# Kernel tuning notes

Measured on AMD Instinct MI355X. Metric: run time of the kernel, lower is better.

Reference implementation:

```python
import jax, jax.numpy as jnp
import numpy as np

BATCH, SEQ, D_MODEL, D_STATE = 16, 1024, 512, 32
DT_MIN, DT_MAX, DT_FLOOR = 1e-3, 1e-1, 1e-4


def _init_ssm(key):
    k1, k2, k3, k4 = jax.random.split(key, 4)
    scale = 1.0 / np.sqrt(D_STATE)
    z = jax.random.normal(k1, (D_MODEL, D_STATE)) * scale
    A_log = -jnp.exp(z)  # A = exp(A_log) in (0,1)
    B = jax.random.normal(k2, (D_MODEL, D_STATE)) * scale
    C = jax.random.normal(k3, (D_MODEL, D_STATE)) * scale
    log_dt = jax.random.uniform(k4, (D_MODEL,)) * (np.log(DT_MAX) - np.log(DT_MIN)) + np.log(DT_MIN)
    log_dt = jnp.maximum(log_dt, np.log(DT_FLOOR))
    return A_log, B, C, log_dt


def setup_inputs() -> dict:
    key = jax.random.key(0)
    kx, khr, kbr = jax.random.split(key, 3)
    x = jax.random.normal(kx, (BATCH, SEQ, D_MODEL), dtype=jnp.float32)
    A_log_hr, B_hr, C_hr, log_dt_hr = _init_ssm(khr)
    A_log_br, B_br, C_br, log_dt_br = _init_ssm(kbr)
    return dict(
        x=x,
        A_log_hr=A_log_hr, B_hr=B_hr, C_hr=C_hr, log_dt_hr=log_dt_hr,
        A_log_br=A_log_br, B_br=B_br, C_br=C_br, log_dt_br=log_dt_br,
        weight_hr=jnp.ones((D_MODEL,), jnp.float32),
        weight_br=jnp.ones((D_MODEL,), jnp.float32),
    )


def _ssm(x, A_log, B, C, log_dt):
    # delta=None path: dt = exp(log_dt) * dt_scale(=1), time-invariant -> dA, dB are [d, n]
    dt = jnp.exp(log_dt)                 # [d]
    A = jnp.exp(A_log)                   # [d, n]
    dA = jnp.exp(dt[:, None] * A)        # [d, n]  (matches torch: exp(dt*exp(A_log)))
    dB = dt[:, None] * B                 # [d, n]
    b = x.shape[0]
    h0 = jnp.zeros((b, A.shape[0], A.shape[1]), x.dtype)  # [b, d, n]

    def step(h, xt):  # xt: [b, d]
        h = dA * h + dB * xt[:, :, None]
        y = jnp.einsum('bdn,dn->bd', h, C)
        return h, y

    _, ys = jax.lax.scan(step, h0, jnp.swapaxes(x, 0, 1))  # ys: [L, b, d]
    return jnp.swapaxes(ys, 0, 1)        # [b, L, d]


def reference(x, A_log_hr, B_hr, C_hr, log_dt_hr,
              A_log_br, B_br, C_br, log_dt_br,
              weight_hr, weight_br):
    x_hr = _ssm(x, A_log_hr, B_hr, C_hr, log_dt_hr) * weight_hr  # [b, L, d]
    x_br = _ssm(x, A_log_br, B_br, C_br, log_dt_br) * weight_br
    return (x_hr, x_br, x_hr + x_br)  # hr_enhanced, br_enhanced, combined
```

## Files before the change

kernel.cpp:

```cpp
#include <hip/hip_runtime.h>

#define BATCH 16
#define SEQ   1024
#define DM    512
#define NST   32
#define PF    8

#define PIN(v) asm volatile("" : "+v"(v))


__global__ __launch_bounds__(256) void ssm_pass1(
    const float* __restrict__ x,
    const float* __restrict__ Alog_hr, const float* __restrict__ ldt_hr,
    const float* __restrict__ Alog_br, const float* __restrict__ ldt_br,
    float* __restrict__ E, int nc, int cl)
{
    int tid  = threadIdx.x;
    int dlo  = tid & 127;
    int nh   = tid >> 7;
    int bid  = blockIdx.x;
    int dblk = bid & 3;
    int r    = bid >> 2;
    int ncm1 = nc - 1;
    int c    = r % ncm1;  r /= ncm1;
    int b    = r & (BATCH - 1);
    int ssm  = r >> 4;
    int d    = dblk * 128 + dlo;
    int n0   = nh * 16;

    const float* Alog = ssm ? Alog_br : Alog_hr;
    const float* ldt  = ssm ? ldt_br  : ldt_hr;

    float dt = expf(ldt[d]);
    float dA[16], g[16];
#pragma unroll
    for (int i = 0; i < 16; ++i) {
        dA[i] = expf(dt * expf(Alog[d * NST + n0 + i]));
        g[i]  = 0.f;
    }
#pragma unroll
    for (int i = 0; i < 16; ++i) PIN(dA[i]);

    const float* xp = x + ((size_t)b * SEQ + (size_t)c * cl) * DM + d;

    float xf[PF];
#pragma unroll
    for (int k = 0; k < PF; ++k) xf[k] = xp[(size_t)k * DM];
    const float* xq = xp + (size_t)PF * DM;

    int ntb = cl / PF;
    for (int t8 = 0; t8 < ntb - 1; ++t8) {
#pragma unroll
        for (int j = 0; j < PF; ++j) {
            float xv = xf[j];
            xf[j] = xq[(size_t)j * DM];
#pragma unroll
            for (int i = 0; i < 16; ++i) g[i] = fmaf(dA[i], g[i], xv);
        }
        xq += (size_t)PF * DM;
    }
#pragma unroll
    for (int j = 0; j < PF; ++j) {
        float xv = xf[j];
#pragma unroll
        for (int i = 0; i < 16; ++i) g[i] = fmaf(dA[i], g[i], xv);
    }

    float* sp = E + ((((size_t)ssm * BATCH + b) * nc + c) * NST + n0) * DM + d;
#pragma unroll
    for (int i = 0; i < 16; ++i) sp[(size_t)i * DM] = g[i];
}

__global__ __launch_bounds__(128, 2) void ssm_pass3(
    const float* __restrict__ x,
    const float* __restrict__ Alog_hr, const float* __restrict__ B_hr,
    const float* __restrict__ C_hr,    const float* __restrict__ ldt_hr,
    const float* __restrict__ Alog_br, const float* __restrict__ B_br,
    const float* __restrict__ C_br,    const float* __restrict__ ldt_br,
    const float* __restrict__ w_hr,    const float* __restrict__ w_br,
    const float* __restrict__ E,
    float* __restrict__ out_hr, float* __restrict__ out_br, float* __restrict__ out_cb,
    int nc, int cl)
{
    int tid  = threadIdx.x;
    int lane = tid & 63;
    int wid  = tid >> 6;
    int ssm  = lane >> 5;
    int dlo  = lane & 31;
    int bid  = blockIdx.x;
    int dblk = bid & 7;
    int r    = bid >> 3;
    int c    = r % nc;
    int b    = r / nc;
    int d    = dblk * 64 + wid * 32 + dlo;

    const float* Alog = ssm ? Alog_br : Alog_hr;
    const float* Bm   = ssm ? B_br    : B_hr;
    const float* Cm   = ssm ? C_br    : C_hr;
    const float* ldt  = ssm ? ldt_br  : ldt_hr;
    const float* w    = ssm ? w_br    : w_hr;

    float dt = expf(ldt[d]);
    float wd = w[d];

    float A[NST], g[NST];
#pragma unroll
    for (int n = 0; n < NST; ++n) {
        A[n] = expf(Alog[d * NST + n]);
        g[n] = 0.f;
    }
    {
        float p[NST];
#pragma unroll
        for (int n = 0; n < NST; ++n) p[n] = expf((float)cl * dt * A[n]);
        const size_t slab = (size_t)NST * DM;
        const float* ep = E + (((size_t)ssm * BATCH + b) * nc) * slab + d;
        for (int cc = 0; cc < c; ++cc) {
#pragma unroll
            for (int n = 0; n < NST; ++n)
                g[n] = fmaf(p[n], g[n], ep[(size_t)n * DM]);
            ep += slab;
        }
    }

    float dA[NST], Cw[NST];
#pragma unroll
    for (int n = 0; n < NST; ++n) {
        dA[n] = expf(dt * A[n]);
        Cw[n] = Cm[d * NST + n] * Bm[d * NST + n] * dt * wd;
    }
#pragma unroll
    for (int n = 0; n < NST; ++n) { PIN(dA[n]); PIN(Cw[n]); }

    size_t off = ((size_t)b * SEQ + (size_t)c * cl) * DM + d;
    const float* xp = x + off;
    float* oh = out_hr + off;
    float* ob = out_br + off;
    float* oc = out_cb + off;

    float xf[PF];
#pragma unroll
    for (int k = 0; k < PF; ++k) xf[k] = xp[(size_t)k * DM];
    const float* xq = xp + (size_t)PF * DM;

#define BODY(xv)                                                        \
    {                                                                   \
        float y0 = 0.f, y1 = 0.f, y2 = 0.f, y3 = 0.f;                   \
        _Pragma("unroll")                                               \
        for (int n = 0; n < NST; n += 4) {                              \
            g[n]     = fmaf(dA[n],     g[n],     xv);                   \
            g[n + 1] = fmaf(dA[n + 1], g[n + 1], xv);                   \
            g[n + 2] = fmaf(dA[n + 2], g[n + 2], xv);                   \
            g[n + 3] = fmaf(dA[n + 3], g[n + 3], xv);                   \
            y0 = fmaf(Cw[n],     g[n],     y0);                         \
            y1 = fmaf(Cw[n + 1], g[n + 1], y1);                         \
            y2 = fmaf(Cw[n + 2], g[n + 2], y2);                         \
            y3 = fmaf(Cw[n + 3], g[n + 3], y3);                         \
        }                                                               \
        float y  = (y0 + y1) + (y2 + y3);                               \
        float yo = __shfl_xor(y, 32, 64);                               \
        if (ssm == 0) { *oh = y; *oc = y + yo; }                        \
        else          { *ob = y; }                                      \
        oh += DM;  ob += DM;  oc += DM;                                 \
    }

    int ntb = cl / PF;
    for (int t8 = 0; t8 < ntb - 1; ++t8) {
#pragma unroll
        for (int j = 0; j < PF; ++j) {
            float xv = xf[j];
            xf[j] = xq[(size_t)j * DM];
            BODY(xv);
        }
        xq += (size_t)PF * DM;
    }
#pragma unroll
    for (int j = 0; j < PF; ++j) {
        float xv = xf[j];
        BODY(xv);
    }
#undef BODY
}

extern "C" void kernel_launch(void* const* d_in, const int* in_sizes, int n_in,
                              void* d_out, int out_size, void* d_ws, size_t ws_size,
                              hipStream_t stream)
{
    (void)in_sizes; (void)n_in; (void)out_size;

    const float* x       = (const float*)d_in[0];
    const float* Alog_hr = (const float*)d_in[1];
    const float* B_hr    = (const float*)d_in[2];
    const float* C_hr    = (const float*)d_in[3];
    const float* ldt_hr  = (const float*)d_in[4];
    const float* Alog_br = (const float*)d_in[5];
    const float* B_br    = (const float*)d_in[6];
    const float* C_br    = (const float*)d_in[7];
    const float* ldt_br  = (const float*)d_in[8];
    const float* w_hr    = (const float*)d_in[9];
    const float* w_br    = (const float*)d_in[10];

    float* out    = (float*)d_out;
    const size_t one = (size_t)BATCH * SEQ * DM;
    float* out_hr = out;
    float* out_br = out + one;
    float* out_cb = out + 2 * one;

    float* E = (float*)d_ws;

    int nc = 8;
    while (nc > 1 &&
           ws_size < (size_t)2 * BATCH * nc * NST * DM * sizeof(float))
        nc >>= 1;
    int cl = SEQ / nc;

    if (nc > 1) {
        int nblk1 = 2 * BATCH * (nc - 1) * 4;
        ssm_pass1<<<nblk1, 256, 0, stream>>>(x, Alog_hr, ldt_hr, Alog_br, ldt_br,
                                             E, nc, cl);
    }

    int nblk3 = BATCH * nc * 8;
    ssm_pass3<<<nblk3, 128, 0, stream>>>(x,
                                         Alog_hr, B_hr, C_hr, ldt_hr,
                                         Alog_br, B_br, C_br, ldt_br,
                                         w_hr, w_br, E,
                                         out_hr, out_br, out_cb, nc, cl);
}
```

Baseline: 74.76 us.

## Add a separate inter-chunk prefix-scan kernel instead of per-block carry recomputation

Adds a new kernel between the chunk-summary pass and the output pass. It runs a sequential scan over the chunk summaries for each (ssm, batch, state, channel) and writes the exclusive prefix state back into the workspace in place. The output pass then loads its starting state with a single read per state. Before, every block recombined all earlier chunks itself, which repeated work and made late chunks slower than early ones. The cost is an extra kernel launch and one more read-write sweep over the workspace.

```diff
diff --git a/kernel.cpp b/kernel.cpp
--- a/kernel.cpp
+++ b/kernel.cpp
@@ -71,6 +71,36 @@
     for (int i = 0; i < 16; ++i) sp[(size_t)i * DM] = g[i];
 }
 
+__global__ __launch_bounds__(256) void ssm_pass2(
+    const float* __restrict__ Alog_hr, const float* __restrict__ ldt_hr,
+    const float* __restrict__ Alog_br, const float* __restrict__ ldt_br,
+    float* __restrict__ E, int nc, int cl)
+{
+    int idx = blockIdx.x * blockDim.x + threadIdx.x;
+    int d   = idx & (DM - 1);
+    int n   = (idx >> 9) & (NST - 1);
+    int b   = (idx >> 14) & 15;
+    int ssm = idx >> 18;
+
+    const float* Alog = ssm ? Alog_br : Alog_hr;
+    const float* ldt  = ssm ? ldt_br  : ldt_hr;
+
+    float dt = expf(ldt[d]);
+    float A  = expf(Alog[d * NST + n]);
+    float p  = expf((float)cl * dt * A);
+
+    float* sp = E + ((((size_t)ssm * BATCH + b) * nc) * NST + n) * DM + d;
+    size_t cstride = (size_t)NST * DM;
+
+    float H = 0.f;
+    for (int c = 0; c < nc; ++c) {
+        float s = *sp;
+        *sp = H;
+        H = fmaf(p, H, s);
+        sp += cstride;
+    }
+}
+
 __global__ __launch_bounds__(128, 2) void ssm_pass3(
     const float* __restrict__ x,
     const float* __restrict__ Alog_hr, const float* __restrict__ B_hr,
@@ -103,34 +133,24 @@
     float dt = expf(ldt[d]);
     float wd = w[d];
 
-    float A[NST], g[NST];
+    float dA[NST], Cw[NST];
 #pragma unroll
     for (int n = 0; n < NST; ++n) {
-        A[n] = expf(Alog[d * NST + n]);
-        g[n] = 0.f;
-    }
-    {
-        float p[NST];
-#pragma unroll
-        for (int n = 0; n < NST; ++n) p[n] = expf((float)cl * dt * A[n]);
-        const size_t slab = (size_t)NST * DM;
-        const float* ep = E + (((size_t)ssm * BATCH + b) * nc) * slab + d;
-        for (int cc = 0; cc < c; ++cc) {
-#pragma unroll
-            for (int n = 0; n < NST; ++n)
-                g[n] = fmaf(p[n], g[n], ep[(size_t)n * DM]);
-            ep += slab;
-        }
-    }
-
-    float dA[NST], Cw[NST];
-#pragma unroll
-    for (int n = 0; n < NST; ++n) {
-        dA[n] = expf(dt * A[n]);
+        dA[n] = expf(dt * expf(Alog[d * NST + n]));
         Cw[n] = Cm[d * NST + n] * Bm[d * NST + n] * dt * wd;
     }
 #pragma unroll
     for (int n = 0; n < NST; ++n) { PIN(dA[n]); PIN(Cw[n]); }
+
+    float g[NST];
+    if (c == 0) {
+#pragma unroll
+        for (int n = 0; n < NST; ++n) g[n] = 0.f;
+    } else {
+        const float* sp = E + ((((size_t)ssm * BATCH + b) * nc + c) * NST) * DM + d;
+#pragma unroll
+        for (int n = 0; n < NST; ++n) g[n] = sp[(size_t)n * DM];
+    }
 
     size_t off = ((size_t)b * SEQ + (size_t)c * cl) * DM + d;
     const float* xp = x + off;
@@ -218,6 +238,9 @@
         int nblk1 = 2 * BATCH * (nc - 1) * 4;
         ssm_pass1<<<nblk1, 256, 0, stream>>>(x, Alog_hr, ldt_hr, Alog_br, ldt_br,
                                              E, nc, cl);
+        int total2 = 2 * BATCH * NST * DM;
+        ssm_pass2<<<total2 / 256, 256, 0, stream>>>(Alog_hr, ldt_hr, Alog_br, ldt_br,
+                                                    E, nc, cl);
     }
 
     int nblk3 = BATCH * nc * 8;
```

Result: slower. 79.00 us (+5.7%).
